# Kernel tuning notes

Hardware: AMD Instinct MI355X
Metric: run time of the kernel (lower is better)

The kernel has to match this reference:

```python
import jax, jax.numpy as jnp
import numpy as np

# dims (match init_kwargs / input_specs)
D = 768      # embed_dim
H = 12       # num query heads
G = 4        # num kv groups
E = 8        # num experts
K = 2        # experts per token
F = 4 * D    # ffn hidden dim
B, S, T = 2, 1024, 1024
DH = D // H  # head dim = 64
EPS = 1e-6


def setup_inputs() -> dict:
    key = jax.random.key(0)
    ks = jax.random.split(key, 16)

    def p(k, shape, scale=0.02):
        return jax.random.normal(k, shape, jnp.float32) * scale

    inp = {}
    inp['x'] = jax.random.normal(ks[0], (B, S, D), jnp.float32)
    inp['encoder_context'] = jax.random.normal(ks[1], (B, T, D), jnp.float32)
    for n in ('ln1', 'ln2', 'ln3'):
        inp[n + '_scale'] = jnp.ones((D,), jnp.float32)
        inp[n + '_bias'] = jnp.zeros((D,), jnp.float32)
    i = 2
    for pre in ('sa', 'ca'):
        inp[pre + '_wq'] = p(ks[i], (D, H * DH)); i += 1
        inp[pre + '_bq'] = jnp.zeros((H * DH,), jnp.float32)
        inp[pre + '_wk'] = p(ks[i], (D, G * DH)); i += 1
        inp[pre + '_bk'] = jnp.zeros((G * DH,), jnp.float32)
        inp[pre + '_wv'] = p(ks[i], (D, G * DH)); i += 1
        inp[pre + '_bv'] = jnp.zeros((G * DH,), jnp.float32)
        inp[pre + '_wo'] = p(ks[i], (H * DH, D)); i += 1
        inp[pre + '_bo'] = jnp.zeros((D,), jnp.float32)
    inp['gate_w'] = p(ks[i], (D, E)); i += 1
    inp['gate_b'] = jnp.zeros((E,), jnp.float32)
    inp['w1'] = p(ks[i], (E, D, F)); i += 1
    inp['b1'] = jnp.zeros((E, F), jnp.float32)
    inp['w2'] = p(ks[i], (E, F, D)); i += 1
    inp['b2'] = jnp.zeros((E, D), jnp.float32)
    return inp


def _ln(x, scale, bias):
    mu = jnp.mean(x, axis=-1, keepdims=True)
    var = jnp.mean(jnp.square(x - mu), axis=-1, keepdims=True)
    return (x - mu) * jax.lax.rsqrt(var + EPS) * scale + bias


def _gqa(q_in, kv_in, wq, bq, wk, bk, wv, bv, wo, bo, causal):
    Bq, Sq, _ = q_in.shape
    Skv = kv_in.shape[1]
    q = (q_in @ wq + bq).reshape(Bq, Sq, H, DH)
    k = (kv_in @ wk + bk).reshape(Bq, Skv, G, DH)
    v = (kv_in @ wv + bv).reshape(Bq, Skv, G, DH)
    rep = H // G
    k = jnp.repeat(k, rep, axis=2)  # [B,Skv,H,DH]
    v = jnp.repeat(v, rep, axis=2)
    scores = jnp.einsum('bqhd,bkhd->bhqk', q, k) / jnp.sqrt(jnp.asarray(DH, q.dtype))
    if causal:
        cmask = jnp.tril(jnp.ones((Sq, Skv), bool))
        scores = jnp.where(cmask[None, None], scores, jnp.finfo(scores.dtype).min)
    attn = jax.nn.softmax(scores, axis=-1)
    out = jnp.einsum('bhqk,bkhd->bqhd', attn, v).reshape(Bq, Sq, H * DH)
    return out @ wo + bo


def _moe(x, gate_w, gate_b, w1, b1, w2, b2):
    logits = x @ gate_w + gate_b                      # [B,S,E]
    probs = jax.nn.softmax(logits, axis=-1)
    top_v, top_i = jax.lax.top_k(probs, K)            # [B,S,K]
    top_v = top_v / jnp.sum(top_v, axis=-1, keepdims=True)
    combine = jnp.sum(jax.nn.one_hot(top_i, E, dtype=x.dtype) * top_v[..., None], axis=-2)  # [B,S,E]
    h = jax.nn.gelu(jnp.einsum('bsd,edf->ebsf', x, w1) + b1[:, None, None, :])
    y = jnp.einsum('ebsf,efd->ebsd', h, w2) + b2[:, None, None, :]
    return jnp.einsum('ebsd,bse->bsd', y, combine)


def reference(x, encoder_context,
              ln1_scale, ln1_bias, ln2_scale, ln2_bias, ln3_scale, ln3_bias,
              sa_wq, sa_bq, sa_wk, sa_bk, sa_wv, sa_bv, sa_wo, sa_bo,
              ca_wq, ca_bq, ca_wk, ca_bk, ca_wv, ca_bv, ca_wo, ca_bo,
              gate_w, gate_b, w1, b1, w2, b2):
    xn = _ln(x, ln1_scale, ln1_bias)
    x = x + _gqa(xn, xn, sa_wq, sa_bq, sa_wk, sa_bk, sa_wv, sa_bv, sa_wo, sa_bo, causal=True)
    xn = _ln(x, ln2_scale, ln2_bias)
    x = x + _gqa(xn, encoder_context, ca_wq, ca_bq, ca_wk, ca_bk, ca_wv, ca_bv, ca_wo, ca_bo, causal=False)
    xn = _ln(x, ln3_scale, ln3_bias)
    x = x + _moe(xn, gate_w, gate_b, w1, b1, w2, b2)
    return x
```

## Files before the change

kernel.cpp:

```cpp
#include <hip/hip_runtime.h>

#define DEV __device__ __forceinline__

typedef __attribute__((ext_vector_type(4))) float f32x4;
typedef __attribute__((ext_vector_type(8))) short short8;
typedef __attribute__((ext_vector_type(4))) unsigned int u32x4;
typedef __attribute__((ext_vector_type(4))) unsigned short us16x4;

#define D_ 768
#define S_ 1024
#define B_ 2
#define H_ 12
#define G_ 4
#define DH_ 64
#define E_ 8
#define F_ 3072
#define NTOK (B_*S_)

DEV unsigned short f2bf(float f){
  unsigned int b = __float_as_uint(f);
  b += 0x7FFFu + ((b >> 16) & 1u);
  return (unsigned short)(b >> 16);
}
DEV float bf2f(unsigned short h){ return __uint_as_float(((unsigned int)h) << 16); }
DEV unsigned int splitbf_pack(float v){
  unsigned short h = f2bf(v);
  unsigned short l = f2bf(v - bf2f(h));
  return (unsigned int)h | ((unsigned int)l << 16);
}

DEV void swz_decode(int F, int nPanels, int& m, int& panel){
  int xcd = F & 7;
  int a = F >> 3;
  int mi = a & 3;
  int pid = (a >> 2)*8 + xcd;
  m = (pid / nPanels)*4 + mi;
  panel = pid % nPanels;
}

__global__ __launch_bounds__(256) void tcast_kernel(const float* __restrict__ W,
                                                    unsigned short* __restrict__ Wh,
                                                    unsigned short* __restrict__ Wl,
                                                    int K, int N){
  __shared__ float tile[32][33];
  long long zoff = (long long)blockIdx.z * K * N;
  const float* Wz = W + zoff;
  int n0 = blockIdx.x*32, k0 = blockIdx.y*32;
  int tx = threadIdx.x, ty = threadIdx.y;
  #pragma unroll
  for (int i=0;i<4;i++){
    int r = ty + i*8;
    tile[r][tx] = Wz[(long long)(k0+r)*N + n0 + tx];
  }
  __syncthreads();
  #pragma unroll
  for (int i=0;i<4;i++){
    int r = ty + i*8;
    float v = tile[tx][r];
    unsigned int hl = splitbf_pack(v);
    long long o = zoff + (long long)(n0+r)*K + k0 + tx;
    Wh[o] = (unsigned short)(hl & 0xFFFFu);
    if (Wl) Wl[o] = (unsigned short)(hl >> 16);
  }
}

__global__ void split_rows(const float* __restrict__ in, int ld, int width,
                           unsigned short* __restrict__ hi, unsigned short* __restrict__ lo){
  long long t = blockIdx.x;
  int c = threadIdx.x*4;
  f32x4 v = *(const f32x4*)(in + t*ld + c);
  unsigned int p0 = splitbf_pack(v.x), p1 = splitbf_pack(v.y);
  unsigned int p2 = splitbf_pack(v.z), p3 = splitbf_pack(v.w);
  us16x4 h, l;
  h.x=(unsigned short)p0; l.x=(unsigned short)(p0>>16);
  h.y=(unsigned short)p1; l.y=(unsigned short)(p1>>16);
  h.z=(unsigned short)p2; l.z=(unsigned short)(p2>>16);
  h.w=(unsigned short)p3; l.w=(unsigned short)(p3>>16);
  *(us16x4*)(hi + t*width + c) = h;
  *(us16x4*)(lo + t*width + c) = l;
}

__global__ void concat_bias(const float* __restrict__ b0, int n0,
                            const float* __restrict__ b1, int n1,
                            const float* __restrict__ b2, int n2,
                            float* __restrict__ out){
  int i = blockIdx.x*256 + threadIdx.x;
  if (i < n0) out[i] = b0[i];
  else if (i < n0+n1) out[i] = b1[i-n0];
  else if (i < n0+n1+n2) out[i] = b2[i-n0-n1];
}

__global__ __launch_bounds__(256) void ln_kernel(const float* __restrict__ x,
                                                 const float* __restrict__ sc,
                                                 const float* __restrict__ bi,
                                                 unsigned short* __restrict__ outh,
                                                 unsigned short* __restrict__ outl,
                                                 float* __restrict__ outf){
  __shared__ float red[8];
  long long row = blockIdx.x;
  const float* xr = x + row*D_;
  int tid = threadIdx.x;
  float v0 = xr[tid], v1 = xr[tid+256], v2 = xr[tid+512];
  float s = v0+v1+v2;
  float q = v0*v0 + v1*v1 + v2*v2;
  #pragma unroll
  for (int off=32; off; off>>=1){ s += __shfl_xor(s, off); q += __shfl_xor(q, off); }
  int lane = tid & 63, w = tid >> 6;
  if (lane == 0){ red[w] = s; red[4+w] = q; }
  __syncthreads();
  s = red[0]+red[1]+red[2]+red[3];
  q = red[4]+red[5]+red[6]+red[7];
  float mu  = s * (1.0f/D_);
  float var = q * (1.0f/D_) - mu*mu;
  float rstd = rsqrtf(var + 1e-6f);
  #pragma unroll
  for (int i=0;i<3;i++){
    int idx = tid + 256*i;
    float vv = (i==0) ? v0 : (i==1) ? v1 : v2;
    float o = (vv - mu)*rstd*sc[idx] + bi[idx];
    unsigned int pk = splitbf_pack(o);
    outh[row*D_ + idx] = (unsigned short)(pk & 0xFFFFu);
    if (outl) outl[row*D_ + idx] = (unsigned short)(pk >> 16);
    if (outf) outf[row*D_ + idx] = o;
  }
}

#define LDK 80
__global__ __launch_bounds__(256) void gemm3(
    int nX,
    const unsigned short* __restrict__ Ah, const unsigned short* __restrict__ Al, int lda,
    const unsigned short* __restrict__ Wh, const unsigned short* __restrict__ Wl, int K,
    const float* __restrict__ bias,
    const float* __restrict__ resid, int ldr,
    float* __restrict__ Cf, int ldc)
{
  __shared__ __align__(16) unsigned short AshH[128*LDK];
  __shared__ __align__(16) unsigned short AshL[128*LDK];
  __shared__ __align__(16) unsigned short BshH[64*LDK];
  __shared__ __align__(16) unsigned short BshL[64*LDK];
  int mB, panel;
  swz_decode(blockIdx.x, nX, mB, panel);
  const int r0 = mB*128;
  const int n0 = panel*64;
  const int tid = threadIdx.x;
  const int lane = tid & 63;
  const int wv = tid >> 6;
  const int wr = (wv>>1)*64, wc = (wv&1)*32;
  const int l15 = lane & 15, l4 = lane >> 4;

  f32x4 acc[4][2];
  #pragma unroll
  for (int i=0;i<4;i++)
    #pragma unroll
    for (int j=0;j<2;j++) acc[i][j] = (f32x4){0.f,0.f,0.f,0.f};

  for (int k0 = 0; k0 < K; k0 += 64){
    #pragma unroll
    for (int i=0;i<4;i++){
      int c = tid + i*256;
      int rr = c >> 3, kc = (c & 7)*8;
      long long src = (long long)(r0+rr)*lda + k0 + kc;
      *(u32x4*)&AshH[rr*LDK+kc] = *(const u32x4*)(Ah + src);
      *(u32x4*)&AshL[rr*LDK+kc] = *(const u32x4*)(Al + src);
    }
    #pragma unroll
    for (int i=0;i<2;i++){
      int c = tid + i*256;
      int rr = c >> 3, kc = (c & 7)*8;
      long long src = (long long)(n0+rr)*K + k0 + kc;
      *(u32x4*)&BshH[rr*LDK+kc] = *(const u32x4*)(Wh + src);
      *(u32x4*)&BshL[rr*LDK+kc] = *(const u32x4*)(Wl + src);
    }
    __syncthreads();
    #pragma unroll
    for (int ks=0; ks<2; ks++){
      int koff = ks*32 + l4*8;
      short8 bh[2], bl[2];
      #pragma unroll
      for (int fj=0; fj<2; fj++){
        bh[fj] = *(const short8*)&BshH[(wc + fj*16 + l15)*LDK + koff];
        bl[fj] = *(const short8*)&BshL[(wc + fj*16 + l15)*LDK + koff];
      }
      #pragma unroll
      for (int fi=0; fi<4; fi++){
        short8 ah = *(const short8*)&AshH[(wr + fi*16 + l15)*LDK + koff];
        short8 al = *(const short8*)&AshL[(wr + fi*16 + l15)*LDK + koff];
        #pragma unroll
        for (int fj=0; fj<2; fj++){
          acc[fi][fj] = __builtin_amdgcn_mfma_f32_16x16x32_bf16(ah, bh[fj], acc[fi][fj], 0,0,0);
          acc[fi][fj] = __builtin_amdgcn_mfma_f32_16x16x32_bf16(al, bh[fj], acc[fi][fj], 0,0,0);
          acc[fi][fj] = __builtin_amdgcn_mfma_f32_16x16x32_bf16(ah, bl[fj], acc[fi][fj], 0,0,0);
        }
      }
    }
    __syncthreads();
  }

  #pragma unroll
  for (int fi=0; fi<4; fi++)
  #pragma unroll
  for (int fj=0; fj<2; fj++)
  #pragma unroll
  for (int reg=0; reg<4; reg++){
    int r = r0 + wr + fi*16 + l4*4 + reg;
    int col = n0 + wc + fj*16 + l15;
    float val = acc[fi][fj][reg] + bias[col];
    if (resid) val += resid[(long long)r*ldr + col];
    Cf[(long long)r*ldc + col] = val;
  }
}

__global__ __launch_bounds__(256) void gemm_nt128(
    int nX, int nzPerE,
    const unsigned short* __restrict__ A, int lda,
    const unsigned short* __restrict__ Wt, long long wstride,
    const float* __restrict__ bias, int bias_stride,
    const int* __restrict__ counts,
    const int* __restrict__ a_idx, int a_idx_stride,
    const int* __restrict__ row_base,
    float* __restrict__ Cf, long long partStride,
    unsigned short* __restrict__ Cb, int ldc,
    int K, int do_gelu)
{
  __shared__ __align__(16) unsigned short As[128*LDK];
  __shared__ __align__(16) unsigned short Bs[128*LDK];
  int mB, panel;
  swz_decode(blockIdx.x, nX*E_*nzPerE, mB, panel);
  const int n0 = (panel % nX)*128;
  const int zI = panel / nX;
  const int z = zI / nzPerE;
  const int kp = zI % nzPerE;
  const int Mz = counts[z];
  const int r0 = mB*128;
  if (r0 >= Mz) return;
  const int obase = row_base[z];
  const unsigned short* Wz = Wt + (long long)z*wstride;
  const float* bz = bias + (long long)z*bias_stride;
  const int kLen = K / nzPerE;
  const int kBeg = kp * kLen;
  const int tid = threadIdx.x;
  const int lane = tid & 63;
  const int wv = tid >> 6;
  const int wr = (wv>>1)*64, wc = (wv&1)*64;
  const int l15 = lane & 15, l4 = lane >> 4;

  long long arow[4];
  #pragma unroll
  for (int i=0;i<4;i++){
    int c = tid + i*256;
    int rr = c >> 3;
    int r = r0 + rr;
    int rcl = (r < Mz) ? r : (Mz-1);
    arow[i] = a_idx ? (long long)a_idx[(long long)z*a_idx_stride + rcl]
                    : (long long)(obase + rcl);
  }

  f32x4 acc[4][4];
  #pragma unroll
  for (int i=0;i<4;i++)
    #pragma unroll
    for (int j=0;j<4;j++) acc[i][j] = (f32x4){0.f,0.f,0.f,0.f};

  for (int k0 = kBeg; k0 < kBeg + kLen; k0 += 64){
    #pragma unroll
    for (int i=0;i<4;i++){
      int c = tid + i*256;
      int rr = c >> 3, kc = (c & 7)*8;
      *(u32x4*)&As[rr*LDK+kc] = *(const u32x4*)(A + arow[i]*lda + k0 + kc);
      *(u32x4*)&Bs[rr*LDK+kc] = *(const u32x4*)(Wz + (long long)(n0+rr)*K + k0 + kc);
    }
    __syncthreads();
    #pragma unroll
    for (int ks=0; ks<2; ks++){
      int koff = ks*32 + l4*8;
      short8 a[4], b[4];
      #pragma unroll
      for (int f=0; f<4; f++){
        a[f] = *(const short8*)&As[(wr + f*16 + l15)*LDK + koff];
        b[f] = *(const short8*)&Bs[(wc + f*16 + l15)*LDK + koff];
      }
      #pragma unroll
      for (int fi=0; fi<4; fi++)
        #pragma unroll
        for (int fj=0; fj<4; fj++)
          acc[fi][fj] = __builtin_amdgcn_mfma_f32_16x16x32_bf16(a[fi], b[fj], acc[fi][fj], 0,0,0);
    }
    __syncthreads();
  }

  #pragma unroll
  for (int fi=0; fi<4; fi++)
  #pragma unroll
  for (int fj=0; fj<4; fj++)
  #pragma unroll
  for (int reg=0; reg<4; reg++){
    int r = r0 + wr + fi*16 + l4*4 + reg;
    if (r >= Mz) continue;
    int col = n0 + wc + fj*16 + l15;
    float val = acc[fi][fj][reg] + (kp == 0 ? bz[col] : 0.0f);
    if (do_gelu){
      float xx = val;
      float u = 0.7978845608028654f*(xx + 0.044715f*xx*xx*xx);
      float t = 1.0f - 2.0f/(__expf(2.0f*u) + 1.0f);
      val = 0.5f*xx*(1.0f + t);
    }
    long long orow = (long long)obase + r;
    if (Cf) Cf[kp*partStride + orow*ldc + col] = val;
    if (Cb) Cb[orow*ldc + col] = f2bf(val);
  }
}

__global__ __launch_bounds__(256) void vt_split_kernel(const float* __restrict__ vin,
                                                       int ld, int cofs,
                                                       unsigned short* __restrict__ vth,
                                                       unsigned short* __restrict__ vtl){
  __shared__ float tile[32][33];
  int s0 = blockIdx.x*32, d0 = blockIdx.y*32;
  int bg = blockIdx.z; int b = bg >> 2, g = bg & 3;
  int tx = threadIdx.x, ty = threadIdx.y;
  #pragma unroll
  for (int i=0;i<4;i++){
    int r = ty + i*8;
    tile[r][tx] = vin[(long long)(b*1024 + s0 + r)*ld + cofs + g*64 + d0 + tx];
  }
  __syncthreads();
  #pragma unroll
  for (int i=0;i<4;i++){
    int d = d0 + ty + i*8;
    unsigned int pk = splitbf_pack(tile[tx][ty + i*8]);
    long long o = (long long)(bg*64 + d)*1024 + s0 + tx;
    vth[o] = (unsigned short)(pk & 0xFFFFu);
    vtl[o] = (unsigned short)(pk >> 16);
  }
}

#define AT_LDK 72
#define AT_LDP 76
__global__ __launch_bounds__(256, 2) void attn_mfma(
    const float* __restrict__ q, int qld,
    const unsigned short* __restrict__ kh, const unsigned short* __restrict__ kl,
    const unsigned short* __restrict__ vth, const unsigned short* __restrict__ vtl,
    unsigned short* __restrict__ ctxh, unsigned short* __restrict__ ctxl, int causal)
{
  __shared__ __align__(16) unsigned short KhS[64*AT_LDK];
  __shared__ __align__(16) unsigned short KlS[64*AT_LDK];
  __shared__ __align__(16) unsigned short VhS[64*AT_LDK];
  __shared__ __align__(16) unsigned short VlS[64*AT_LDK];
  __shared__ __align__(16) unsigned int   Pp[4][16*AT_LDP];

  const int qblk = blockIdx.x;
  const int h = blockIdx.y;
  const int b = blockIdx.z;
  const int g = h / (H_/G_);
  const int tid = threadIdx.x;
  const int lane = tid & 63;
  const int w = tid >> 6;
  const int l15 = lane & 15;
  const int l4 = lane >> 4;
  const int qb0 = qblk*64;

  short8 qh[2], ql[2];
  #pragma unroll
  for (int ks=0; ks<2; ks++){
    const float* qp = q + ((long long)(b*S_ + qb0 + w*16 + l15))*qld + h*DH_ + ks*32 + l4*8;
    f32x4 q0 = *(const f32x4*)qp;
    f32x4 q1 = *(const f32x4*)(qp + 4);
    float qq[8] = {q0.x,q0.y,q0.z,q0.w,q1.x,q1.y,q1.z,q1.w};
    #pragma unroll
    for (int j=0;j<8;j++){
      unsigned int pk = splitbf_pack(qq[j]*0.125f);
      qh[ks][j] = (short)(pk & 0xFFFFu);
      ql[ks][j] = (short)(pk >> 16);
    }
  }

  f32x4 o[4];
  #pragma unroll
  for (int fd=0; fd<4; fd++) o[fd] = (f32x4){0.f,0.f,0.f,0.f};
  float m[4]    = {-3.0e38f,-3.0e38f,-3.0e38f,-3.0e38f};
  float lsum[4] = {0.f,0.f,0.f,0.f};

  const int ntiles = causal ? (qblk + 1) : (S_/64);
  for (int kt=0; kt<ntiles; kt++){
    __syncthreads();
    {
      int r = tid >> 2, c = tid & 3;
      long long krow = (long long)(b*S_ + kt*64 + r)*(G_*DH_) + g*DH_;
      long long vrow = (long long)((b*G_ + g)*64 + r)*S_ + kt*64;
      *(u32x4*)&KhS[r*AT_LDK + c*8]     = *(const u32x4*)(kh + krow + c*8);
      *(u32x4*)&KhS[r*AT_LDK + (c+4)*8] = *(const u32x4*)(kh + krow + (c+4)*8);
      *(u32x4*)&KlS[r*AT_LDK + c*8]     = *(const u32x4*)(kl + krow + c*8);
      *(u32x4*)&KlS[r*AT_LDK + (c+4)*8] = *(const u32x4*)(kl + krow + (c+4)*8);
      *(u32x4*)&VhS[r*AT_LDK + c*8]     = *(const u32x4*)(vth + vrow + c*8);
      *(u32x4*)&VhS[r*AT_LDK + (c+4)*8] = *(const u32x4*)(vth + vrow + (c+4)*8);
      *(u32x4*)&VlS[r*AT_LDK + c*8]     = *(const u32x4*)(vtl + vrow + c*8);
      *(u32x4*)&VlS[r*AT_LDK + (c+4)*8] = *(const u32x4*)(vtl + vrow + (c+4)*8);
    }
    __syncthreads();

    f32x4 s[4];
    #pragma unroll
    for (int fj=0; fj<4; fj++) s[fj] = (f32x4){0.f,0.f,0.f,0.f};
    #pragma unroll
    for (int ks=0; ks<2; ks++){
      #pragma unroll
      for (int fj=0; fj<4; fj++){
        short8 bh = *(const short8*)&KhS[(fj*16 + l15)*AT_LDK + ks*32 + l4*8];
        short8 bl = *(const short8*)&KlS[(fj*16 + l15)*AT_LDK + ks*32 + l4*8];
        s[fj] = __builtin_amdgcn_mfma_f32_16x16x32_bf16(qh[ks], bh, s[fj], 0,0,0);
        s[fj] = __builtin_amdgcn_mfma_f32_16x16x32_bf16(ql[ks], bh, s[fj], 0,0,0);
        s[fj] = __builtin_amdgcn_mfma_f32_16x16x32_bf16(qh[ks], bl, s[fj], 0,0,0);
      }
    }

    if (causal && kt == qblk){
      #pragma unroll
      for (int fj=0; fj<4; fj++){
        int key = kt*64 + fj*16 + l15;
        #pragma unroll
        for (int reg=0; reg<4; reg++){
          int qr = qb0 + w*16 + l4*4 + reg;
          if (key > qr) s[fj][reg] = -3.0e38f;
        }
      }
    }

    float c[4], pmax[4];
    #pragma unroll
    for (int reg=0; reg<4; reg++){
      float mx = fmaxf(fmaxf(s[0][reg], s[1][reg]), fmaxf(s[2][reg], s[3][reg]));
      mx = fmaxf(mx, __shfl_xor(mx, 1));
      mx = fmaxf(mx, __shfl_xor(mx, 2));
      mx = fmaxf(mx, __shfl_xor(mx, 4));
      mx = fmaxf(mx, __shfl_xor(mx, 8));
      float mn = fmaxf(m[reg], mx);
      c[reg] = __expf(m[reg] - mn);
      m[reg] = mn;
      pmax[reg] = mn;
    }
    float psum[4] = {0.f,0.f,0.f,0.f};
    #pragma unroll
    for (int fj=0; fj<4; fj++){
      #pragma unroll
      for (int reg=0; reg<4; reg++){
        float pv = __expf(s[fj][reg] - pmax[reg]);
        psum[reg] += pv;
        Pp[w][(l4*4 + reg)*AT_LDP + fj*16 + l15] = splitbf_pack(pv);
      }
    }
    #pragma unroll
    for (int reg=0; reg<4; reg++){
      float ps = psum[reg];
      ps += __shfl_xor(ps, 1); ps += __shfl_xor(ps, 2);
      ps += __shfl_xor(ps, 4); ps += __shfl_xor(ps, 8);
      lsum[reg] = lsum[reg]*c[reg] + ps;
      o[0][reg] *= c[reg]; o[1][reg] *= c[reg];
      o[2][reg] *= c[reg]; o[3][reg] *= c[reg];
    }

    #pragma unroll
    for (int ks=0; ks<2; ks++){
      u32x4 pa = *(const u32x4*)&Pp[w][l15*AT_LDP + ks*32 + l4*8];
      u32x4 pb = *(const u32x4*)&Pp[w][l15*AT_LDP + ks*32 + l4*8 + 4];
      short8 ph, pl;
      #pragma unroll
      for (int j=0;j<4;j++){
        ph[j]   = (short)(pa[j] & 0xFFFFu); pl[j]   = (short)(pa[j] >> 16);
        ph[4+j] = (short)(pb[j] & 0xFFFFu); pl[4+j] = (short)(pb[j] >> 16);
      }
      #pragma unroll
      for (int fd=0; fd<4; fd++){
        short8 vh = *(const short8*)&VhS[(fd*16 + l15)*AT_LDK + ks*32 + l4*8];
        short8 vl = *(const short8*)&VlS[(fd*16 + l15)*AT_LDK + ks*32 + l4*8];
        o[fd] = __builtin_amdgcn_mfma_f32_16x16x32_bf16(ph, vh, o[fd], 0,0,0);
        o[fd] = __builtin_amdgcn_mfma_f32_16x16x32_bf16(pl, vh, o[fd], 0,0,0);
        o[fd] = __builtin_amdgcn_mfma_f32_16x16x32_bf16(ph, vl, o[fd], 0,0,0);
      }
    }
  }

  #pragma unroll
  for (int reg=0; reg<4; reg++){
    float inv = 1.0f / lsum[reg];
    long long tok = b*S_ + qb0 + w*16 + l4*4 + reg;
    #pragma unroll
    for (int fd=0; fd<4; fd++){
      unsigned int pk = splitbf_pack(o[fd][reg]*inv);
      long long oidx = tok*D_ + h*DH_ + fd*16 + l15;
      ctxh[oidx] = (unsigned short)(pk & 0xFFFFu);
      ctxl[oidx] = (unsigned short)(pk >> 16);
    }
  }
}

__global__ __launch_bounds__(256) void gate_kernel(const float* __restrict__ xnf,
                                                   const float* __restrict__ gw,
                                                   const float* __restrict__ gb,
                                                   int* __restrict__ counts,
                                                   int* __restrict__ toklist,
                                                   int* __restrict__ route_e,
                                                   int* __restrict__ route_pos,
                                                   float* __restrict__ route_w){
  int t = blockIdx.x*4 + (threadIdx.x >> 6);
  int lane = threadIdx.x & 63;
  float acc[E_];
  #pragma unroll
  for (int e=0;e<E_;e++) acc[e] = 0.f;
  #pragma unroll
  for (int i=0;i<12;i++){
    int d = lane + 64*i;
    float xv = xnf[(long long)t*D_ + d];
    const float* w = gw + (long long)d*E_;
    #pragma unroll
    for (int e=0;e<E_;e++) acc[e] += xv*w[e];
  }
  #pragma unroll
  for (int off=32; off; off>>=1)
    #pragma unroll
    for (int e=0;e<E_;e++) acc[e] += __shfl_xor(acc[e], off);
  if (lane == 0){
    #pragma unroll
    for (int e=0;e<E_;e++) acc[e] += gb[e];
    int e0 = 0;
    #pragma unroll
    for (int e=1;e<E_;e++) if (acc[e] > acc[e0]) e0 = e;
    int e1 = -1;
    #pragma unroll
    for (int e=0;e<E_;e++) if (e != e0 && (e1 < 0 || acc[e] > acc[e1])) e1 = e;
    float w0 = 1.0f/(1.0f + __expf(acc[e1] - acc[e0]));
    float w1 = 1.0f - w0;
    int p0 = atomicAdd(&counts[e0], 1);
    int p1 = atomicAdd(&counts[e1], 1);
    toklist[e0*NTOK + p0] = t;
    toklist[e1*NTOK + p1] = t;
    route_e[2*t]   = e0; route_e[2*t+1]   = e1;
    route_pos[2*t] = p0; route_pos[2*t+1] = p1;
    route_w[2*t]   = w0; route_w[2*t+1]   = w1;
  }
}

__global__ void offsets_kernel(const int* __restrict__ counts, int* __restrict__ offs){
  if (threadIdx.x == 0){
    int s = 0;
    for (int e=0;e<E_;e++){ offs[e] = s; s += counts[e]; }
  }
}

__global__ __launch_bounds__(192) void combine_kernel(const float* __restrict__ xb,
                                                      const float* __restrict__ y,
                                                      long long partStride,
                                                      const int* __restrict__ route_e,
                                                      const int* __restrict__ route_pos,
                                                      const float* __restrict__ route_w,
                                                      const int* __restrict__ offs,
                                                      float* __restrict__ out){
  int t = blockIdx.x;
  int i = threadIdx.x;
  int e0 = route_e[2*t], e1 = route_e[2*t+1];
  long long s0 = offs[e0] + route_pos[2*t];
  long long s1 = offs[e1] + route_pos[2*t+1];
  float w0 = route_w[2*t], w1 = route_w[2*t+1];
  f32x4 xv  = *(const f32x4*)(xb + (long long)t*D_ + i*4);
  f32x4 y0a = *(const f32x4*)(y + s0*D_ + i*4);
  f32x4 y0b = *(const f32x4*)(y + partStride + s0*D_ + i*4);
  f32x4 y1a = *(const f32x4*)(y + s1*D_ + i*4);
  f32x4 y1b = *(const f32x4*)(y + partStride + s1*D_ + i*4);
  f32x4 o = xv + w0*(y0a + y0b) + w1*(y1a + y1b);
  *(f32x4*)(out + (long long)t*D_ + i*4) = o;
}

extern "C" void kernel_launch(void* const* d_in, const int* in_sizes, int n_in,
                              void* d_out, int out_size, void* d_ws, size_t ws_size,
                              hipStream_t stream) {
  (void)in_sizes; (void)n_in; (void)out_size; (void)ws_size;
  const float* x     = (const float*)d_in[0];
  const float* enc   = (const float*)d_in[1];
  const float* ln1s  = (const float*)d_in[2];
  const float* ln1b  = (const float*)d_in[3];
  const float* ln2s  = (const float*)d_in[4];
  const float* ln2b  = (const float*)d_in[5];
  const float* ln3s  = (const float*)d_in[6];
  const float* ln3b  = (const float*)d_in[7];
  const float* sa_wq = (const float*)d_in[8];
  const float* sa_bq = (const float*)d_in[9];
  const float* sa_wk = (const float*)d_in[10];
  const float* sa_bk = (const float*)d_in[11];
  const float* sa_wv = (const float*)d_in[12];
  const float* sa_bv = (const float*)d_in[13];
  const float* sa_wo = (const float*)d_in[14];
  const float* sa_bo = (const float*)d_in[15];
  const float* ca_wq = (const float*)d_in[16];
  const float* ca_bq = (const float*)d_in[17];
  const float* ca_wk = (const float*)d_in[18];
  const float* ca_bk = (const float*)d_in[19];
  const float* ca_wv = (const float*)d_in[20];
  const float* ca_bv = (const float*)d_in[21];
  const float* ca_wo = (const float*)d_in[22];
  const float* ca_bo = (const float*)d_in[23];
  const float* gate_w= (const float*)d_in[24];
  const float* gate_b= (const float*)d_in[25];
  const float* w1    = (const float*)d_in[26];
  const float* b1    = (const float*)d_in[27];
  const float* w2    = (const float*)d_in[28];
  const float* b2    = (const float*)d_in[29];
  float* out = (float*)d_out;

  char* p = (char*)d_ws;
  auto alloc = [&](size_t bytes)->void*{
    void* r = (void*)p;
    p += (bytes + 255) & ~(size_t)255;
    return r;
  };
  unsigned short* wqkvh_sa = (unsigned short*)alloc((size_t)1280*768*2);
  unsigned short* wqkvl_sa = (unsigned short*)alloc((size_t)1280*768*2);
  unsigned short* woh_sa   = (unsigned short*)alloc((size_t)768*768*2);
  unsigned short* wol_sa   = (unsigned short*)alloc((size_t)768*768*2);
  unsigned short* wqh_ca   = (unsigned short*)alloc((size_t)768*768*2);
  unsigned short* wql_ca   = (unsigned short*)alloc((size_t)768*768*2);
  unsigned short* wkvh_ca  = (unsigned short*)alloc((size_t)512*768*2);
  unsigned short* wkvl_ca  = (unsigned short*)alloc((size_t)512*768*2);
  unsigned short* woh_ca   = (unsigned short*)alloc((size_t)768*768*2);
  unsigned short* wol_ca   = (unsigned short*)alloc((size_t)768*768*2);
  unsigned short* w1T = (unsigned short*)alloc((size_t)E_*D_*F_*2);
  unsigned short* w2T = (unsigned short*)alloc((size_t)E_*D_*F_*2);
  float* bqkv_sa = (float*)alloc(1280*4);
  float* bkv_ca  = (float*)alloc(512*4);
  unsigned short* ench = (unsigned short*)alloc((size_t)NTOK*D_*2);
  unsigned short* encl = (unsigned short*)alloc((size_t)NTOK*D_*2);
  unsigned short* xh   = (unsigned short*)alloc((size_t)NTOK*D_*2);
  unsigned short* xl   = (unsigned short*)alloc((size_t)NTOK*D_*2);
  unsigned short* ctxh = (unsigned short*)alloc((size_t)NTOK*D_*2);
  unsigned short* ctxl = (unsigned short*)alloc((size_t)NTOK*D_*2);
  unsigned short* xn_b = (unsigned short*)alloc((size_t)NTOK*D_*2);
  unsigned short* hbuf = (unsigned short*)alloc((size_t)2*NTOK*F_*2);
  unsigned short* khp   = (unsigned short*)alloc((size_t)NTOK*G_*DH_*2);
  unsigned short* klp   = (unsigned short*)alloc((size_t)NTOK*G_*DH_*2);
  unsigned short* vtp_h = (unsigned short*)alloc((size_t)NTOK*G_*DH_*2);
  unsigned short* vtp_l = (unsigned short*)alloc((size_t)NTOK*G_*DH_*2);
  float* qkvbuf = (float*)alloc((size_t)NTOK*1280*4);
  float* xnf  = (float*)alloc((size_t)NTOK*D_*4);
  float* xbuf = (float*)alloc((size_t)NTOK*D_*4);
  float* ybuf = (float*)alloc((size_t)4*NTOK*D_*4);
  int* counts    = (int*)alloc(E_*4);
  int* offs      = (int*)alloc(E_*4);
  int* toklist   = (int*)alloc((size_t)E_*NTOK*4);
  int* route_e   = (int*)alloc((size_t)2*NTOK*4);
  int* route_pos = (int*)alloc((size_t)2*NTOK*4);
  float* route_w = (float*)alloc((size_t)2*NTOK*4);

  (void)hipMemsetAsync(counts, 0, E_*sizeof(int), stream);

  dim3 tb(32,8);
  tcast_kernel<<<dim3(24,24,1), tb, 0, stream>>>(sa_wq, wqkvh_sa,            wqkvl_sa,            768, 768);
  tcast_kernel<<<dim3( 8,24,1), tb, 0, stream>>>(sa_wk, wqkvh_sa + 768*768,  wqkvl_sa + 768*768,  768, 256);
  tcast_kernel<<<dim3( 8,24,1), tb, 0, stream>>>(sa_wv, wqkvh_sa + 1024*768, wqkvl_sa + 1024*768, 768, 256);
  tcast_kernel<<<dim3(24,24,1), tb, 0, stream>>>(sa_wo, woh_sa, wol_sa, 768, 768);
  tcast_kernel<<<dim3(24,24,1), tb, 0, stream>>>(ca_wq, wqh_ca, wql_ca, 768, 768);
  tcast_kernel<<<dim3( 8,24,1), tb, 0, stream>>>(ca_wk, wkvh_ca,           wkvl_ca,           768, 256);
  tcast_kernel<<<dim3( 8,24,1), tb, 0, stream>>>(ca_wv, wkvh_ca + 256*768, wkvl_ca + 256*768, 768, 256);
  tcast_kernel<<<dim3(24,24,1), tb, 0, stream>>>(ca_wo, woh_ca, wol_ca, 768, 768);
  tcast_kernel<<<dim3(96,24,E_), tb, 0, stream>>>(w1, w1T, nullptr, 768, 3072);
  tcast_kernel<<<dim3(24,96,E_), tb, 0, stream>>>(w2, w2T, nullptr, 3072, 768);
  concat_bias<<<5, 256, 0, stream>>>(sa_bq, 768, sa_bk, 256, sa_bv, 256, bqkv_sa);
  concat_bias<<<2, 256, 0, stream>>>(ca_bk, 256, ca_bv, 256, nullptr, 0, bkv_ca);
  split_rows<<<NTOK, 192, 0, stream>>>(enc, 768, 768, ench, encl);

  ln_kernel<<<NTOK, 256, 0, stream>>>(x, ln1s, ln1b, xh, xl, nullptr);
  gemm3<<<20*16, 256, 0, stream>>>(20, xh, xl, 768, wqkvh_sa, wqkvl_sa, 768,
      bqkv_sa, nullptr, 0, qkvbuf, 1280);
  split_rows<<<NTOK, 64, 0, stream>>>(qkvbuf + 768, 1280, 256, khp, klp);
  vt_split_kernel<<<dim3(32,2,8), tb, 0, stream>>>(qkvbuf, 1280, 1024, vtp_h, vtp_l);
  attn_mfma<<<dim3(16,12,2), 256, 0, stream>>>(qkvbuf, 1280, khp, klp, vtp_h, vtp_l, ctxh, ctxl, 1);
  gemm3<<<12*16, 256, 0, stream>>>(12, ctxh, ctxl, 768, woh_sa, wol_sa, 768,
      sa_bo, x, 768, xbuf, 768);

  ln_kernel<<<NTOK, 256, 0, stream>>>(xbuf, ln2s, ln2b, xh, xl, nullptr);
  gemm3<<<12*16, 256, 0, stream>>>(12, xh, xl, 768, wqh_ca, wql_ca, 768,
      ca_bq, nullptr, 0, qkvbuf, 1280);
  gemm3<<<8*16, 256, 0, stream>>>(8, ench, encl, 768, wkvh_ca, wkvl_ca, 768,
      bkv_ca, nullptr, 0, qkvbuf + 768, 1280);
  split_rows<<<NTOK, 64, 0, stream>>>(qkvbuf + 768, 1280, 256, khp, klp);
  vt_split_kernel<<<dim3(32,2,8), tb, 0, stream>>>(qkvbuf, 1280, 1024, vtp_h, vtp_l);
  attn_mfma<<<dim3(16,12,2), 256, 0, stream>>>(qkvbuf, 1280, khp, klp, vtp_h, vtp_l, ctxh, ctxl, 0);
  gemm3<<<12*16, 256, 0, stream>>>(12, ctxh, ctxl, 768, woh_ca, wol_ca, 768,
      ca_bo, xbuf, 768, xbuf, 768);

  ln_kernel<<<NTOK, 256, 0, stream>>>(xbuf, ln3s, ln3b, xn_b, nullptr, xnf);
  gate_kernel<<<NTOK/4, 256, 0, stream>>>(xnf, gate_w, gate_b,
      counts, toklist, route_e, route_pos, route_w);
  offsets_kernel<<<1, 64, 0, stream>>>(counts, offs);
  gemm_nt128<<<24*16*E_, 256, 0, stream>>>(24, 1, xn_b, 768, w1T, (long long)F_*D_, b1, F_,
      counts, toklist, NTOK, offs, nullptr, 0, hbuf, F_, 768, 1);
  long long partStride = (long long)2*NTOK*D_;
  gemm_nt128<<<6*16*E_*2, 256, 0, stream>>>(6, 2, hbuf, F_, w2T, (long long)F_*D_, b2, D_,
      counts, nullptr, 0, offs, ybuf, partStride, nullptr, 768, F_, 0);
  combine_kernel<<<NTOK, 192, 0, stream>>>(xbuf, ybuf, partStride,
      route_e, route_pos, route_w, offs, out);
}
```

Baseline: 534.4 us.

## Use direct global-to-LDS loads with XOR swizzle and deepen split-K for FFN2

Both GEMM kernels now stage A and B tiles through global_load_lds, which writes straight into shared memory without passing through registers. The padded LDS layout is replaced by an unpadded 64-column layout with an XOR chunk swizzle to avoid bank conflicts. Separately, the second MoE GEMM is split four ways along K instead of two, and the combine kernel now sums four partial buffers. The split-K change needs a larger partial buffer and more reduction traffic in combine, and it relies on the bias being added only once across partials.

```diff
diff --git a/kernel.cpp b/kernel.cpp
--- a/kernel.cpp
+++ b/kernel.cpp
@@ -17,6 +17,10 @@
 #define F_ 3072
 #define NTOK (B_*S_)
 
+#define GLDS16(g, l) __builtin_amdgcn_global_load_lds( \
+    (const __attribute__((address_space(1))) void*)(g), \
+    (__attribute__((address_space(3))) void*)(l), 16, 0, 0)
+
 DEV unsigned short f2bf(float f){
   unsigned int b = __float_as_uint(f);
   b += 0x7FFFu + ((b >> 16) & 1u);
@@ -29,9 +33,13 @@
   return (unsigned int)h | ((unsigned int)l << 16);
 }
 
-DEV void swz_decode(int F, int nPanels, int& m, int& panel){
-  int xcd = F & 7;
-  int a = F >> 3;
+DEV short8 lds_swz(const unsigned short* base, int row, int chunk){
+  return *(const short8*)((const char*)base + row*128 + (((chunk ^ (row & 7)) << 4)));
+}
+
+DEV void swz_decode(int Fb, int nPanels, int& m, int& panel){
+  int xcd = Fb & 7;
+  int a = Fb >> 3;
   int mi = a & 3;
   int pid = (a >> 2)*8 + xcd;
   m = (pid / nPanels)*4 + mi;
@@ -125,7 +133,6 @@
   }
 }
 
-#define LDK 80
 __global__ __launch_bounds__(256) void gemm3(
     int nX,
     const unsigned short* __restrict__ Ah, const unsigned short* __restrict__ Al, int lda,
@@ -134,10 +141,10 @@
     const float* __restrict__ resid, int ldr,
     float* __restrict__ Cf, int ldc)
 {
-  __shared__ __align__(16) unsigned short AshH[128*LDK];
-  __shared__ __align__(16) unsigned short AshL[128*LDK];
-  __shared__ __align__(16) unsigned short BshH[64*LDK];
-  __shared__ __align__(16) unsigned short BshL[64*LDK];
+  __shared__ __align__(16) unsigned short AshH[128*64];
+  __shared__ __align__(16) unsigned short AshL[128*64];
+  __shared__ __align__(16) unsigned short BshH[64*64];
+  __shared__ __align__(16) unsigned short BshL[64*64];
   int mB, panel;
   swz_decode(blockIdx.x, nX, mB, panel);
   const int r0 = mB*128;
@@ -147,6 +154,8 @@
   const int wv = tid >> 6;
   const int wr = (wv>>1)*64, wc = (wv&1)*32;
   const int l15 = lane & 15, l4 = lane >> 4;
+  const int sr = lane >> 3;
+  const int sc = (lane & 7) ^ sr;
 
   f32x4 acc[4][2];
   #pragma unroll
@@ -157,34 +166,32 @@
   for (int k0 = 0; k0 < K; k0 += 64){
     #pragma unroll
     for (int i=0;i<4;i++){
-      int c = tid + i*256;
-      int rr = c >> 3, kc = (c & 7)*8;
-      long long src = (long long)(r0+rr)*lda + k0 + kc;
-      *(u32x4*)&AshH[rr*LDK+kc] = *(const u32x4*)(Ah + src);
-      *(u32x4*)&AshL[rr*LDK+kc] = *(const u32x4*)(Al + src);
+      int seg = wv*4 + i;
+      long long src = (long long)(r0 + seg*8 + sr)*lda + k0 + sc*8;
+      GLDS16(Ah + src, AshH + seg*8*64);
+      GLDS16(Al + src, AshL + seg*8*64);
     }
     #pragma unroll
     for (int i=0;i<2;i++){
-      int c = tid + i*256;
-      int rr = c >> 3, kc = (c & 7)*8;
-      long long src = (long long)(n0+rr)*K + k0 + kc;
-      *(u32x4*)&BshH[rr*LDK+kc] = *(const u32x4*)(Wh + src);
-      *(u32x4*)&BshL[rr*LDK+kc] = *(const u32x4*)(Wl + src);
+      int seg = wv*2 + i;
+      long long src = (long long)(n0 + seg*8 + sr)*K + k0 + sc*8;
+      GLDS16(Wh + src, BshH + seg*8*64);
+      GLDS16(Wl + src, BshL + seg*8*64);
     }
     __syncthreads();
     #pragma unroll
     for (int ks=0; ks<2; ks++){
-      int koff = ks*32 + l4*8;
+      int chunk = ks*4 + l4;
       short8 bh[2], bl[2];
       #pragma unroll
       for (int fj=0; fj<2; fj++){
-        bh[fj] = *(const short8*)&BshH[(wc + fj*16 + l15)*LDK + koff];
-        bl[fj] = *(const short8*)&BshL[(wc + fj*16 + l15)*LDK + koff];
+        bh[fj] = lds_swz(BshH, wc + fj*16 + l15, chunk);
+        bl[fj] = lds_swz(BshL, wc + fj*16 + l15, chunk);
       }
       #pragma unroll
       for (int fi=0; fi<4; fi++){
-        short8 ah = *(const short8*)&AshH[(wr + fi*16 + l15)*LDK + koff];
-        short8 al = *(const short8*)&AshL[(wr + fi*16 + l15)*LDK + koff];
+        short8 ah = lds_swz(AshH, wr + fi*16 + l15, chunk);
+        short8 al = lds_swz(AshL, wr + fi*16 + l15, chunk);
         #pragma unroll
         for (int fj=0; fj<2; fj++){
           acc[fi][fj] = __builtin_amdgcn_mfma_f32_16x16x32_bf16(ah, bh[fj], acc[fi][fj], 0,0,0);
@@ -222,8 +229,8 @@
     unsigned short* __restrict__ Cb, int ldc,
     int K, int do_gelu)
 {
-  __shared__ __align__(16) unsigned short As[128*LDK];
-  __shared__ __align__(16) unsigned short Bs[128*LDK];
+  __shared__ __align__(16) unsigned short As[128*64];
+  __shared__ __align__(16) unsigned short Bs[128*64];
   int mB, panel;
   swz_decode(blockIdx.x, nX*E_*nzPerE, mB, panel);
   const int n0 = (panel % nX)*128;
@@ -243,13 +250,14 @@
   const int wv = tid >> 6;
   const int wr = (wv>>1)*64, wc = (wv&1)*64;
   const int l15 = lane & 15, l4 = lane >> 4;
+  const int sr = lane >> 3;
+  const int sc = (lane & 7) ^ sr;
 
   long long arow[4];
   #pragma unroll
   for (int i=0;i<4;i++){
-    int c = tid + i*256;
-    int rr = c >> 3;
-    int r = r0 + rr;
+    int seg = wv*4 + i;
+    int r = r0 + seg*8 + sr;
     int rcl = (r < Mz) ? r : (Mz-1);
     arow[i] = a_idx ? (long long)a_idx[(long long)z*a_idx_stride + rcl]
                     : (long long)(obase + rcl);
@@ -264,20 +272,19 @@
   for (int k0 = kBeg; k0 < kBeg + kLen; k0 += 64){
     #pragma unroll
     for (int i=0;i<4;i++){
-      int c = tid + i*256;
-      int rr = c >> 3, kc = (c & 7)*8;
-      *(u32x4*)&As[rr*LDK+kc] = *(const u32x4*)(A + arow[i]*lda + k0 + kc);
-      *(u32x4*)&Bs[rr*LDK+kc] = *(const u32x4*)(Wz + (long long)(n0+rr)*K + k0 + kc);
+      int seg = wv*4 + i;
+      GLDS16(A + arow[i]*lda + k0 + sc*8, As + seg*8*64);
+      GLDS16(Wz + (long long)(n0 + seg*8 + sr)*K + k0 + sc*8, Bs + seg*8*64);
     }
     __syncthreads();
     #pragma unroll
     for (int ks=0; ks<2; ks++){
-      int koff = ks*32 + l4*8;
+      int chunk = ks*4 + l4;
       short8 a[4], b[4];
       #pragma unroll
       for (int f=0; f<4; f++){
-        a[f] = *(const short8*)&As[(wr + f*16 + l15)*LDK + koff];
-        b[f] = *(const short8*)&Bs[(wc + f*16 + l15)*LDK + koff];
+        a[f] = lds_swz(As, wr + f*16 + l15, chunk);
+        b[f] = lds_swz(Bs, wc + f*16 + l15, chunk);
       }
       #pragma unroll
       for (int fi=0; fi<4; fi++)
@@ -560,12 +567,15 @@
   long long s0 = offs[e0] + route_pos[2*t];
   long long s1 = offs[e1] + route_pos[2*t+1];
   float w0 = route_w[2*t], w1 = route_w[2*t+1];
-  f32x4 xv  = *(const f32x4*)(xb + (long long)t*D_ + i*4);
-  f32x4 y0a = *(const f32x4*)(y + s0*D_ + i*4);
-  f32x4 y0b = *(const f32x4*)(y + partStride + s0*D_ + i*4);
-  f32x4 y1a = *(const f32x4*)(y + s1*D_ + i*4);
-  f32x4 y1b = *(const f32x4*)(y + partStride + s1*D_ + i*4);
-  f32x4 o = xv + w0*(y0a + y0b) + w1*(y1a + y1b);
+  f32x4 xv = *(const f32x4*)(xb + (long long)t*D_ + i*4);
+  f32x4 y0 = (f32x4){0.f,0.f,0.f,0.f};
+  f32x4 y1 = (f32x4){0.f,0.f,0.f,0.f};
+  #pragma unroll
+  for (int kp=0; kp<4; kp++){
+    y0 += *(const f32x4*)(y + kp*partStride + s0*D_ + i*4);
+    y1 += *(const f32x4*)(y + kp*partStride + s1*D_ + i*4);
+  }
+  f32x4 o = xv + w0*y0 + w1*y1;
   *(f32x4*)(out + (long long)t*D_ + i*4) = o;
 }
 
@@ -640,7 +650,7 @@
   float* qkvbuf = (float*)alloc((size_t)NTOK*1280*4);
   float* xnf  = (float*)alloc((size_t)NTOK*D_*4);
   float* xbuf = (float*)alloc((size_t)NTOK*D_*4);
-  float* ybuf = (float*)alloc((size_t)4*NTOK*D_*4);
+  float* ybuf = (float*)alloc((size_t)8*NTOK*D_*4);
   int* counts    = (int*)alloc(E_*4);
   int* offs      = (int*)alloc(E_*4);
   int* toklist   = (int*)alloc((size_t)E_*NTOK*4);
@@ -692,7 +702,7 @@
   gemm_nt128<<<24*16*E_, 256, 0, stream>>>(24, 1, xn_b, 768, w1T, (long long)F_*D_, b1, F_,
       counts, toklist, NTOK, offs, nullptr, 0, hbuf, F_, 768, 1);
   long long partStride = (long long)2*NTOK*D_;
-  gemm_nt128<<<6*16*E_*2, 256, 0, stream>>>(6, 2, hbuf, F_, w2T, (long long)F_*D_, b2, D_,
+  gemm_nt128<<<6*16*E_*4, 256, 0, stream>>>(6, 4, hbuf, F_, w2T, (long long)F_*D_, b2, D_,
       counts, nullptr, 0, offs, ybuf, partStride, nullptr, 768, F_, 0);
   combine_kernel<<<NTOK, 192, 0, stream>>>(xbuf, ybuf, partStride,
       route_e, route_pos, route_w, offs, out);
```

New measurement: 514.7 us. 1.04x faster.
